# Kernel optimization log

Measured on AMD Instinct MI355X. Metric: run time of the kernel, lower is better.

Reference implementation:

```python
import jax, jax.numpy as jnp
import numpy as np
from jax import lax

B, T, V, E, H = 256, 512, 128, 64, 256


def lstm_cell(x, h, c, Wih, Whh, bih, bhh):
    # PyTorch gate order: i, f, g, o
    gates = x @ Wih.T + h @ Whh.T + bih + bhh
    i, f, g, o = jnp.split(gates, 4, axis=-1)
    c_new = jax.nn.sigmoid(f) * c + jax.nn.sigmoid(i) * jnp.tanh(g)
    h_new = jax.nn.sigmoid(o) * jnp.tanh(c_new)
    return h_new, c_new


def setup_inputs() -> dict:
    key = jax.random.key(0)
    ks = jax.random.split(key, 16)
    s = 0.05
    emb = jax.random.normal(ks[1], (V, E), jnp.float32) * s
    emb = emb.at[0].set(0.0)  # padding_idx=0
    return {
        "x": jax.random.randint(ks[0], (B, T), 0, V),
        "emb": emb,
        "Wih_e": jax.random.normal(ks[2], (4 * H, E), jnp.float32) * s,
        "Whh_e": jax.random.normal(ks[3], (4 * H, H), jnp.float32) * s,
        "bih_e": jax.random.normal(ks[4], (4 * H,), jnp.float32) * s,
        "bhh_e": jax.random.normal(ks[5], (4 * H,), jnp.float32) * s,
        "Wq": jax.random.normal(ks[6], (H, H), jnp.float32) * s,
        "Wk": jax.random.normal(ks[7], (H, H), jnp.float32) * s,
        "v": jax.random.normal(ks[8], (H,), jnp.float32) * s,
        "Wih_d": jax.random.normal(ks[9], (4 * H, E + H), jnp.float32) * s,
        "Whh_d": jax.random.normal(ks[10], (4 * H, H), jnp.float32) * s,
        "bih_d": jax.random.normal(ks[11], (4 * H,), jnp.float32) * s,
        "bhh_d": jax.random.normal(ks[12], (4 * H,), jnp.float32) * s,
        "Wfc": jax.random.normal(ks[13], (V, H), jnp.float32) * s,
        "bfc": jax.random.normal(ks[14], (V,), jnp.float32) * s,
    }


def reference(x, emb, Wih_e, Whh_e, bih_e, bhh_e, Wq, Wk, v,
              Wih_d, Whh_d, bih_d, bhh_d, Wfc, bfc):
    Bx = x.shape[0]
    embedded = emb[x]                          # (B, T, E)  (dropout in eval mode = identity)
    emb_tbE = embedded.transpose(1, 0, 2)      # (T, B, E)

    # ---- Encoder LSTM ----
    h0 = jnp.zeros((Bx, H), embedded.dtype)
    c0 = jnp.zeros((Bx, H), embedded.dtype)

    def enc_step(carry, x_t):
        h, c = carry
        h, c = lstm_cell(x_t, h, c, Wih_e, Whh_e, bih_e, bhh_e)
        return (h, c), h

    (h_n, c_n), enc_seq = lax.scan(enc_step, (h0, c0), emb_tbE)
    enc_out = enc_seq.transpose(1, 0, 2)       # (B, T, H)

    # ---- Attention precompute ----
    keys_proj = enc_out @ Wk.T                 # (B, T, H)
    pad_mask = (x == 0)                        # (B, T)

    # ---- Decoder loop (teacher forcing) ----
    def dec_step(carry, emb_t):
        h, c = carry
        q = h @ Wq.T                                        # (B, H)
        energy = jnp.tanh(q[:, None, :] + keys_proj) @ v    # (B, T)
        energy = jnp.where(pad_mask, -1e9, energy)
        w = jax.nn.softmax(energy, axis=-1)
        context = jnp.einsum('bt,bth->bh', w, enc_out)      # (B, H)
        dec_in = jnp.concatenate([emb_t, context], axis=-1)  # (B, E+H)
        h, c = lstm_cell(dec_in, h, c, Wih_d, Whh_d, bih_d, bhh_d)
        return (h, c), h

    (h_f, c_f), dec_seq = lax.scan(dec_step, (h_n, c_n), emb_tbE)
    logits = dec_seq.transpose(1, 0, 2) @ Wfc.T + bfc       # (B, T, V)
    return logits, h_f, c_f
```

## Files before the change

### kernel.cpp

```cpp
#include <hip/hip_runtime.h>
#include <hip/hip_bf16.h>
#include <stdint.h>

#define NB 256
#define NT 512
#define NV 128
#define NE 64
#define NH 256

typedef __fp16 h2t __attribute__((ext_vector_type(2)));

__device__ __forceinline__ float lo_bf(unsigned u){ return __uint_as_float(u << 16); }
__device__ __forceinline__ float hi_bf(unsigned u){ return __uint_as_float(u & 0xffff0000u); }
__device__ __forceinline__ unsigned short f2us(float f){
  unsigned u = __float_as_uint(f);
  unsigned r = u + 0x7fffu + ((u >> 16) & 1u);
  return (unsigned short)(r >> 16);
}
__device__ __forceinline__ float sigm(float x){
  return __builtin_amdgcn_rcpf(1.f + __expf(-x));
}
__device__ __forceinline__ float ftanh(float xx){
  float a = fabsf(xx);
  a = fminf(a, 9.f);
  float e = __expf(2.f * a);
  float r = __builtin_amdgcn_rcpf(e + 1.f);
  float t = (e - 1.f) * r;
  return copysignf(t, xx);
}
__device__ __forceinline__ unsigned pkf16(float a, float b){
  h2t h = __builtin_amdgcn_cvt_pkrtz(a, b);
  unsigned u; __builtin_memcpy(&u, &h, 4); return u;
}
__device__ __forceinline__ float fdot2(unsigned a, unsigned b, float c){
#if __has_builtin(__builtin_amdgcn_fdot2)
  h2t A, B; __builtin_memcpy(&A, &a, 4); __builtin_memcpy(&B, &b, 4);
  return __builtin_amdgcn_fdot2(A, B, c, false);
#else
  h2t A, B; __builtin_memcpy(&A, &a, 4); __builtin_memcpy(&B, &b, 4);
  return c + (float)A.x*(float)B.x + (float)A.y*(float)B.y;
#endif
}

__global__ __launch_bounds__(256, 1)
void prep_kernel(const float* __restrict__ Wq, const float* __restrict__ Wfc,
                 const float* __restrict__ Wihd, const float* __restrict__ Whhd,
                 const float* __restrict__ Wihe, const float* __restrict__ Whhe,
                 const float* __restrict__ Wk,
                 unsigned* __restrict__ Wq4, unsigned* __restrict__ Wfc4,
                 unsigned* __restrict__ Wihd4, unsigned* __restrict__ Whhd4,
                 unsigned* __restrict__ Wihe4, unsigned* __restrict__ Whhe4,
                 unsigned* __restrict__ Wke4)
{
  const int blk = blockIdx.x, tid = threadIdx.x;
  if (blk < 64){
    int k2p = blk;
    #pragma unroll
    for (int l = 0; l < 2; ++l){
      int i = l*256 + tid, c = i>>1, j = i&1, k = 4*k2p + 2*j;
      Wq4[k2p*512 + i] = pkf16(Wq[c*256 + k], Wq[c*256 + k + 1]);
    }
  } else if (blk < 128){
    int k2p = blk - 64;
    int c = tid>>1, j = tid&1, k = 4*k2p + 2*j;
    Wfc4[k2p*256 + tid] = pkf16(Wfc[c*256 + k], Wfc[c*256 + k + 1]);
  } else if (blk < 208){
    int k2p = blk - 128;
    #pragma unroll
    for (int l = 0; l < 8; ++l){
      int i = l*256 + tid, g = i>>1, j = i&1, k = 4*k2p + 2*j;
      Wihd4[(size_t)k2p*2048 + i] = pkf16(Wihd[g*320 + k], Wihd[g*320 + k + 1]);
    }
  } else if (blk < 272){
    int k2p = blk - 208;
    #pragma unroll
    for (int l = 0; l < 8; ++l){
      int i = l*256 + tid, g = i>>1, j = i&1, k = 4*k2p + 2*j;
      Whhd4[(size_t)k2p*2048 + i] = pkf16(Whhd[g*256 + k], Whhd[g*256 + k + 1]);
    }
  } else if (blk < 288){
    int k2p = blk - 272;
    #pragma unroll
    for (int l = 0; l < 8; ++l){
      int i = l*256 + tid, g = i>>1, j = i&1, k = 4*k2p + 2*j;
      Wihe4[(size_t)k2p*2048 + i] = pkf16(Wihe[g*64 + k], Wihe[g*64 + k + 1]);
    }
  } else if (blk < 352){
    int k2p = blk - 288;
    #pragma unroll
    for (int l = 0; l < 8; ++l){
      int i = l*256 + tid, g = i>>1, j = i&1, k = 4*k2p + 2*j;
      Whhe4[(size_t)k2p*2048 + i] = pkf16(Whhe[g*256 + k], Whhe[g*256 + k + 1]);
    }
  } else {
    int k2p = blk - 352;
    #pragma unroll
    for (int l = 0; l < 2; ++l){
      int i = l*256 + tid, c = i>>1, j = i&1, k = 4*k2p + 2*j;
      Wke4[k2p*512 + i] = pkf16(Wk[c*256 + k], Wk[c*256 + k + 1]);
    }
  }
}

__global__ __launch_bounds__(256, 1)
void tr_kernel(const unsigned short* __restrict__ keys_n, unsigned short* __restrict__ keys_t)
{
  __shared__ unsigned short tile[64][68];
  const int blk = blockIdx.x, tid = threadIdx.x;
  const int b  = blk >> 5;
  const int tt = (blk >> 2) & 7;
  const int hh = blk & 3;
  const int t0 = tt*64, h0 = hh*64;

  #pragma unroll
  for (int i = 0; i < 4; ++i){
    int idx = tid + i*256;
    int t = idx >> 4, h4 = (idx & 15)*4;
    uint2 u = *(const uint2*)(keys_n + ((size_t)b*NT + t0 + t)*NH + h0 + h4);
    *(uint2*)&tile[t][h4] = u;
  }
  __syncthreads();
  #pragma unroll
  for (int i = 0; i < 4; ++i){
    int idx = tid + i*256;
    int h = idx >> 4, t4 = (idx & 15)*4;
    unsigned short a = tile[t4+0][h], bb = tile[t4+1][h], cc = tile[t4+2][h], dd = tile[t4+3][h];
    uint2 u; u.x = (unsigned)a | ((unsigned)bb << 16); u.y = (unsigned)cc | ((unsigned)dd << 16);
    *(uint2*)(keys_t + ((size_t)b*NH + h0 + h)*NT + t0 + t4) = u;
  }
}

__global__ __launch_bounds__(1024, 1)
void enc_kernel(const int* __restrict__ x, const float* __restrict__ emb,
                const unsigned* __restrict__ Wihe4, const unsigned* __restrict__ Whhe4,
                const float* __restrict__ bih, const float* __restrict__ bhh,
                const unsigned* __restrict__ Wke4,
                unsigned short* __restrict__ enc_out, unsigned short* __restrict__ keys_n,
                float* __restrict__ g_h, float* __restrict__ g_c)
{
  const int tid = threadIdx.x;
  const int b0  = blockIdx.x * 2;

  __shared__ unsigned sH2[2][128];
  __shared__ unsigned sXe2[2][32];
  __shared__ float sG[2][1024];
  __shared__ float sBias[1024];
  __shared__ float sKP[1024];
  __shared__ uint8_t sXi[2][512];

  sBias[tid] = bih[tid] + bhh[tid];
  { int r = tid >> 9; sXi[r][tid & 511] = (uint8_t)x[(b0 + r)*NT + (tid & 511)]; }
  if (tid < 256) sH2[tid>>7][tid&127] = 0u;
  __syncthreads();
  if (tid < 64){
    int r = tid>>5, p = tid&31, idx = sXi[r][0];
    sXe2[r][p] = pkf16(emb[idx*NE + 2*p], emb[idx*NE + 2*p + 1]);
  }
  float creg = 0.f, hl = 0.f;
  __syncthreads();

  for (int t = 0; t < NT; ++t){
    {
      const int g = tid;
      float a0 = sBias[g], a1 = a0;
      const unsigned* Wi = Wihe4 + g*2;
      #pragma unroll 4
      for (int p = 0; p < 16; ++p){
        uint2 w = *(const uint2*)(Wi + (size_t)p*2048);
        a0 = fdot2(sXe2[0][2*p], w.x, a0); a0 = fdot2(sXe2[0][2*p+1], w.y, a0);
        a1 = fdot2(sXe2[1][2*p], w.x, a1); a1 = fdot2(sXe2[1][2*p+1], w.y, a1);
      }
      const unsigned* Wh = Whhe4 + g*2;
      #pragma unroll 4
      for (int p = 0; p < 64; ++p){
        uint2 w = *(const uint2*)(Wh + (size_t)p*2048);
        a0 = fdot2(sH2[0][2*p], w.x, a0); a0 = fdot2(sH2[0][2*p+1], w.y, a0);
        a1 = fdot2(sH2[1][2*p], w.x, a1); a1 = fdot2(sH2[1][2*p+1], w.y, a1);
      }
      sG[0][g] = a0; sG[1][g] = a1;
    }
    if (t > 0){
      const int r = tid>>9, half = (tid>>8)&1, c = tid&255;
      float kp = 0.f;
      const unsigned* Wk4 = Wke4 + c*2;
      #pragma unroll 4
      for (int p = 0; p < 32; ++p){
        int k2p = half*32 + p;
        uint2 w = *(const uint2*)(Wk4 + k2p*512);
        kp = fdot2(sH2[r][2*k2p], w.x, kp);
        kp = fdot2(sH2[r][2*k2p+1], w.y, kp);
      }
      sKP[tid] = kp;
    }
    __syncthreads();
    if (tid < 512){
      const int r = tid>>8, cc = tid&255;
      float gi = sigm (sG[r][cc]);
      float gf = sigm (sG[r][256+cc]);
      float gg = ftanh(sG[r][512+cc]);
      float go = sigm (sG[r][768+cc]);
      float cn = gf*creg + gi*gg;
      float hn = go*ftanh(cn);
      creg = cn; hl = hn;
      enc_out[((size_t)(b0+r)*NT + t)*NH + cc] = f2us(hn);
      float hb = __shfl_down(hn, 1, 64);
      if (!(cc & 1)) sH2[r][cc>>1] = pkf16(hn, hb);
      if (tid < 64 && (t+1) < NT){
        int r2 = tid>>5, p = tid&31, idx = sXi[r2][t+1];
        sXe2[r2][p] = pkf16(emb[idx*NE + 2*p], emb[idx*NE + 2*p + 1]);
      }
    } else if (t > 0){
      const int r = (tid>>8)&1, c = tid&255;
      float kv = sKP[(r<<9) + c] + sKP[(r<<9) + 256 + c];
      keys_n[((size_t)(b0+r)*NT + (t-1))*NH + c] = f2us(kv);
    }
    __syncthreads();
  }
  {
    const int r = tid>>9, half = (tid>>8)&1, c = tid&255;
    float kp = 0.f;
    const unsigned* Wk4 = Wke4 + c*2;
    #pragma unroll 4
    for (int p = 0; p < 32; ++p){
      int k2p = half*32 + p;
      uint2 w = *(const uint2*)(Wk4 + k2p*512);
      kp = fdot2(sH2[r][2*k2p], w.x, kp);
      kp = fdot2(sH2[r][2*k2p+1], w.y, kp);
    }
    sKP[tid] = kp;
  }
  __syncthreads();
  if (tid >= 512){
    const int r = (tid>>8)&1, c = tid&255;
    float kv = sKP[(r<<9) + c] + sKP[(r<<9) + 256 + c];
    keys_n[((size_t)(b0+r)*NT + (NT-1))*NH + c] = f2us(kv);
  } else {
    const int r = tid>>8, cc = tid&255;
    g_h[(b0+r)*NH + cc] = hl;
    g_c[(b0+r)*NH + cc] = creg;
  }
}

__global__ __launch_bounds__(1024, 1)
void dec_kernel(const int* __restrict__ x, const float* __restrict__ emb,
                const unsigned* __restrict__ Wq4, const float* __restrict__ vvec,
                const unsigned* __restrict__ Wihd4, const unsigned* __restrict__ Whhd4,
                const float* __restrict__ bih, const float* __restrict__ bhh,
                const unsigned short* __restrict__ enc_out, const unsigned short* __restrict__ keys_t,
                const float* __restrict__ g_h, const float* __restrict__ g_c,
                unsigned* __restrict__ h2_hist, float* __restrict__ out_h, float* __restrict__ out_c)
{
  const int tid = threadIdx.x;
  const int b   = blockIdx.x;

  extern __shared__ unsigned short sKpin[];

  __shared__ float sTMP[4096];
  __shared__ float sWp[512];
  __shared__ float sRed[8];
  __shared__ float sQ2[256];
  __shared__ unsigned sH2[128];
  __shared__ unsigned sCtx2[128];
  __shared__ unsigned sXe2[32];
  __shared__ float sG[1024];
  __shared__ float sBiasD[1024];
  __shared__ float sVm2[256];
  __shared__ float sVs[8];
  __shared__ uint8_t sXi[512];

  sBiasD[tid] = bih[tid] + bhh[tid];
  if (tid < 256) sVm2[tid] = -2.f * vvec[tid];
  if (tid < 512) sXi[tid] = (uint8_t)x[b*NT + tid];
  if (tid < 128) sH2[tid] = pkf16(g_h[b*NH + 2*tid], g_h[b*NH + 2*tid + 1]);
  if (tid < 8){
    float s = 0.f;
    #pragma unroll
    for (int j = 0; j < 12; ++j) s += vvec[tid*12 + j];
    #pragma unroll
    for (int j = 0; j < 20; ++j) s += vvec[96 + tid*20 + j];
    sVs[tid] = s;
  }
  {
    const unsigned* src = (const unsigned*)(keys_t + (size_t)b*NH*NT);
    unsigned* dst = (unsigned*)sKpin;
    #pragma unroll
    for (int i = 0; i < 24; ++i) dst[tid + i*1024] = src[tid + i*1024];
  }
  float creg = (tid < 256) ? g_c[b*NH + tid] : 0.f;
  float hl = 0.f;
  const float CLN = 2.885390081777927f;
  __syncthreads();

  for (int t = 0; t < NT; ++t){
    {
      const int c = tid & 255, kq = tid >> 8;
      float a = 0.f;
      const unsigned* Wp = Wq4 + c*2;
      #pragma unroll 4
      for (int p = 0; p < 16; ++p){
        int k2p = kq*16 + p;
        uint2 w = *(const uint2*)(Wp + k2p*512);
        a = fdot2(sH2[2*k2p], w.x, a);
        a = fdot2(sH2[2*k2p+1], w.y, a);
      }
      sTMP[kq*256 + c] = a;
    }
    __syncthreads();
    if (tid < 256){
      float qv = sTMP[tid] + sTMP[256 + tid] + sTMP[512 + tid] + sTMP[768 + tid];
      sQ2[tid] = CLN * qv;
    } else if (tid < 288){
      int p = tid - 256, idx = sXi[t];
      sXe2[p] = pkf16(emb[idx*NE + 2*p], emb[idx*NE + 2*p + 1]);
    }
    __syncthreads();
    {
      const int kh = tid >> 7, sp = tid & 127;
      float e0 = sVs[kh], e1 = e0, e2 = e0, e3 = e0;
      const unsigned short* ktg = keys_t + ((size_t)b*NH + 96 + kh*20)*NT + sp*4;
      #pragma unroll 4
      for (int j = 0; j < 20; ++j){
        uint2 u = *(const uint2*)(ktg + (size_t)j*NT);
        int ka = 96 + kh*20 + j;
        float q2 = sQ2[ka];
        float vm = sVm2[ka];
        float r0 = __builtin_amdgcn_rcpf(1.f + exp2f(fmaf(CLN, lo_bf(u.x), q2)));
        float r1 = __builtin_amdgcn_rcpf(1.f + exp2f(fmaf(CLN, hi_bf(u.x), q2)));
        float r2 = __builtin_amdgcn_rcpf(1.f + exp2f(fmaf(CLN, lo_bf(u.y), q2)));
        float r3 = __builtin_amdgcn_rcpf(1.f + exp2f(fmaf(CLN, hi_bf(u.y), q2)));
        e0 = fmaf(vm, r0, e0); e1 = fmaf(vm, r1, e1);
        e2 = fmaf(vm, r2, e2); e3 = fmaf(vm, r3, e3);
      }
      const unsigned short* ktl = sKpin + (size_t)(kh*12)*NT + sp*4;
      #pragma unroll 4
      for (int j = 0; j < 12; ++j){
        uint2 u = *(const uint2*)(ktl + (size_t)j*NT);
        int ka = kh*12 + j;
        float q2 = sQ2[ka];
        float vm = sVm2[ka];
        float r0 = __builtin_amdgcn_rcpf(1.f + exp2f(fmaf(CLN, lo_bf(u.x), q2)));
        float r1 = __builtin_amdgcn_rcpf(1.f + exp2f(fmaf(CLN, hi_bf(u.x), q2)));
        float r2 = __builtin_amdgcn_rcpf(1.f + exp2f(fmaf(CLN, lo_bf(u.y), q2)));
        float r3 = __builtin_amdgcn_rcpf(1.f + exp2f(fmaf(CLN, hi_bf(u.y), q2)));
        e0 = fmaf(vm, r0, e0); e1 = fmaf(vm, r1, e1);
        e2 = fmaf(vm, r2, e2); e3 = fmaf(vm, r3, e3);
      }
      *(float4*)(sTMP + kh*512 + sp*4) = make_float4(e0,e1,e2,e3);
    }
    __syncthreads();
    if (tid < 512){
      float e = sTMP[tid]      + sTMP[512+tid]  + sTMP[1024+tid] + sTMP[1536+tid]
              + sTMP[2048+tid] + sTMP[2560+tid] + sTMP[3072+tid] + sTMP[3584+tid];
      float w = (sXi[tid] == 0) ? 0.f : __expf(e);
      sWp[tid] = w;
      float s = w;
      #pragma unroll
      for (int off = 32; off > 0; off >>= 1) s += __shfl_down(s, off, 64);
      if ((tid & 63) == 0) sRed[tid >> 6] = s;
    }
    __syncthreads();
    {
      const int sc = tid >> 6;
      const int kc = tid & 63;
      const unsigned short* ep = enc_out + ((size_t)b*NT + sc*32)*NH + kc*4;
      float a0=0.f, a1=0.f, a2=0.f, a3=0.f;
      #pragma unroll 8
      for (int ss = 0; ss < 32; ++ss){
        float w = sWp[sc*32 + ss];
        uint2 u = *(const uint2*)(ep + (size_t)ss*NH);
        a0 += w*lo_bf(u.x); a1 += w*hi_bf(u.x);
        a2 += w*lo_bf(u.y); a3 += w*hi_bf(u.y);
      }
      *(float4*)(sTMP + sc*256 + kc*4) = make_float4(a0,a1,a2,a3);
    }
    __syncthreads();
    if (tid < 256){
      float den = sRed[0]+sRed[1]+sRed[2]+sRed[3]+sRed[4]+sRed[5]+sRed[6]+sRed[7];
      float rden = (den > 0.f) ? (1.f/den) : 0.f;
      float cs = 0.f;
      #pragma unroll
      for (int p = 0; p < 16; ++p) cs += sTMP[p*256 + tid];
      float cv = cs * rden;
      float cb = __shfl_down(cv, 1, 64);
      if (!(tid & 1)) sCtx2[tid>>1] = pkf16(cv, cb);
    }
    __syncthreads();
    {
      const int g = tid;
      float a = sBiasD[g];
      const unsigned* Wi = Wihd4 + g*2;
      #pragma unroll 4
      for (int p = 0; p < 16; ++p){
        uint2 w = *(const uint2*)(Wi + (size_t)p*2048);
        a = fdot2(sXe2[2*p], w.x, a); a = fdot2(sXe2[2*p+1], w.y, a);
      }
      #pragma unroll 4
      for (int p = 0; p < 64; ++p){
        uint2 w = *(const uint2*)(Wi + (size_t)(16+p)*2048);
        a = fdot2(sCtx2[2*p], w.x, a); a = fdot2(sCtx2[2*p+1], w.y, a);
      }
      const unsigned* Wh = Whhd4 + g*2;
      #pragma unroll 4
      for (int p = 0; p < 64; ++p){
        uint2 w = *(const uint2*)(Wh + (size_t)p*2048);
        a = fdot2(sH2[2*p], w.x, a); a = fdot2(sH2[2*p+1], w.y, a);
      }
      sG[g] = a;
    }
    __syncthreads();
    if (tid < 256){
      float gi = sigm (sG[tid]);
      float gf = sigm (sG[256 + tid]);
      float gg = ftanh(sG[512 + tid]);
      float go = sigm (sG[768 + tid]);
      float cn = gf*creg + gi*gg;
      float hn = go*ftanh(cn);
      creg = cn; hl = hn;
      float hb = __shfl_down(hn, 1, 64);
      if (!(tid & 1)){
        unsigned hp = pkf16(hn, hb);
        sH2[tid>>1] = hp;
        h2_hist[((size_t)b*NT + t)*128 + (tid>>1)] = hp;
      }
    }
    __syncthreads();
  }

  if (tid < 256){
    out_h[b*NH + tid] = hl;
    out_c[b*NH + tid] = creg;
  }
}

__global__ __launch_bounds__(256, 1)
void fc_kernel(const unsigned* __restrict__ h2_hist, const unsigned* __restrict__ Wfc4,
               const float* __restrict__ bfc, float* __restrict__ logits)
{
  __shared__ unsigned sHH[1024];
  const int tid = threadIdx.x;
  const size_t row0 = (size_t)blockIdx.x * 8;
  #pragma unroll
  for (int l = 0; l < 4; ++l) sHH[l*256 + tid] = h2_hist[row0*128 + l*256 + tid];
  __syncthreads();
  const int r = tid >> 7, v = tid & 127;
  float bv = bfc[v];
  float a0 = bv, a1 = bv, a2 = bv, a3 = bv;
  const unsigned* Wp = Wfc4 + v*2;
  #pragma unroll 4
  for (int k2p = 0; k2p < 64; ++k2p){
    uint2 w = *(const uint2*)(Wp + k2p*256);
    int k2 = 2*k2p;
    a0 = fdot2(sHH[(r  )*128 + k2], w.x, a0); a0 = fdot2(sHH[(r  )*128 + k2+1], w.y, a0);
    a1 = fdot2(sHH[(r+2)*128 + k2], w.x, a1); a1 = fdot2(sHH[(r+2)*128 + k2+1], w.y, a1);
    a2 = fdot2(sHH[(r+4)*128 + k2], w.x, a2); a2 = fdot2(sHH[(r+4)*128 + k2+1], w.y, a2);
    a3 = fdot2(sHH[(r+6)*128 + k2], w.x, a3); a3 = fdot2(sHH[(r+6)*128 + k2+1], w.y, a3);
  }
  logits[(row0 + r    )*NV + v] = a0;
  logits[(row0 + r + 2)*NV + v] = a1;
  logits[(row0 + r + 4)*NV + v] = a2;
  logits[(row0 + r + 6)*NV + v] = a3;
}

extern "C" void kernel_launch(void* const* d_in, const int* in_sizes, int n_in,
                              void* d_out, int out_size, void* d_ws, size_t ws_size,
                              hipStream_t stream)
{
  (void)in_sizes; (void)n_in; (void)out_size; (void)ws_size;
  const int*   x    = (const int*)  d_in[0];
  const float* emb  = (const float*)d_in[1];
  const float* Wihe = (const float*)d_in[2];
  const float* Whhe = (const float*)d_in[3];
  const float* bihe = (const float*)d_in[4];
  const float* bhhe = (const float*)d_in[5];
  const float* Wq   = (const float*)d_in[6];
  const float* Wk   = (const float*)d_in[7];
  const float* vv   = (const float*)d_in[8];
  const float* Wihd = (const float*)d_in[9];
  const float* Whhd = (const float*)d_in[10];
  const float* bihd = (const float*)d_in[11];
  const float* bhhd = (const float*)d_in[12];
  const float* Wfc  = (const float*)d_in[13];
  const float* bfc  = (const float*)d_in[14];

  char* ws = (char*)d_ws;
  const size_t M64 = 67108864;
  unsigned short* enc   = (unsigned short*)(ws);
  unsigned short* keysn = (unsigned short*)(ws + M64);
  unsigned short* keyst = (unsigned short*)(ws + 2*M64);
  unsigned* h2_hist     = (unsigned*)(ws + M64);
  float* g_h = (float*)(ws + 3*M64);
  float* g_c = g_h + NB*NH;
  unsigned* Wq4   = (unsigned*)(g_c + NB*NH);
  unsigned* Wfc4  = Wq4   + 64*512;
  unsigned* Wihd4 = Wfc4  + 64*256;
  unsigned* Whhd4 = Wihd4 + 80*2048;
  unsigned* Wihe4 = Whhd4 + 64*2048;
  unsigned* Whhe4 = Wihe4 + 16*2048;
  unsigned* Wke4  = Whhe4 + 64*2048;

  float* out_logits = (float*)d_out;
  float* out_h = out_logits + (size_t)NB*NT*NV;
  float* out_c = out_h + NB*NH;

  const int dynLds = 96 * 512 * 2;
  static int attrSet = 0;
  if (!attrSet){
    hipFuncSetAttribute(reinterpret_cast<const void*>(dec_kernel),
                        hipFuncAttributeMaxDynamicSharedMemorySize, dynLds);
    attrSet = 1;
  }

  prep_kernel<<<dim3(416), dim3(256), 0, stream>>>(
      Wq, Wfc, Wihd, Whhd, Wihe, Whhe, Wk,
      Wq4, Wfc4, Wihd4, Whhd4, Wihe4, Whhe4, Wke4);
  enc_kernel<<<dim3(128), dim3(1024), 0, stream>>>(
      x, emb, Wihe4, Whhe4, bihe, bhhe, Wke4, enc, keysn, g_h, g_c);
  tr_kernel<<<dim3(8192), dim3(256), 0, stream>>>(keysn, keyst);
  dec_kernel<<<dim3(256), dim3(1024), dynLds, stream>>>(
      x, emb, Wq4, vv, Wihd4, Whhd4, bihd, bhhd,
      enc, keyst, g_h, g_c, h2_hist, out_h, out_c);
  fc_kernel<<<dim3(16384), dim3(256), 0, stream>>>(h2_hist, Wfc4, bfc, out_logits);
}
```

Before: 25.47 ms.

## Split decoder threads to overlap recurrent-gate matvec with attention phases

Threads 0-511 now compute the attention energies and context with 8-wide vector loads, instead of all 1024 threads doing 4-wide work. The other 512 threads compute the h·Whh and embedding·Wih parts of the gate pre-activations into a new shared buffer during those same phases. The final gate stage then only needs the context·Wih part. This hides the h-dependent matvec behind attention work and shortens the serial gate phase, at the cost of halving the threads available for the attention math.

After: 25.86 ms. Within noise of the previous version (+1.5%).

```diff
diff --git a/kernel.cpp b/kernel.cpp
--- a/kernel.cpp
+++ b/kernel.cpp
@@ -256,6 +256,7 @@
   extern __shared__ unsigned short sKpin[];
 
   __shared__ float sTMP[4096];
+  __shared__ float sGP[1024];
   __shared__ float sWp[512];
   __shared__ float sRed[8];
   __shared__ float sQ2[256];
@@ -292,6 +293,7 @@
   __syncthreads();
 
   for (int t = 0; t < NT; ++t){
+    float ga0 = 0.f, ga1 = 0.f;
     {
       const int c = tid & 255, kq = tid >> 8;
       float a = 0.f;
@@ -314,38 +316,50 @@
       sXe2[p] = pkf16(emb[idx*NE + 2*p], emb[idx*NE + 2*p + 1]);
     }
     __syncthreads();
-    {
-      const int kh = tid >> 7, sp = tid & 127;
-      float e0 = sVs[kh], e1 = e0, e2 = e0, e3 = e0;
-      const unsigned short* ktg = keys_t + ((size_t)b*NH + 96 + kh*20)*NT + sp*4;
-      #pragma unroll 4
+    if (tid < 512){
+      const int kh = tid >> 6, sp = tid & 63;
+      float e0 = sVs[kh], e1 = e0, e2 = e0, e3 = e0, e4 = e0, e5 = e0, e6 = e0, e7 = e0;
+      const unsigned short* ktg = keys_t + ((size_t)b*NH + 96 + kh*20)*NT + sp*8;
+      #pragma unroll 2
       for (int j = 0; j < 20; ++j){
-        uint2 u = *(const uint2*)(ktg + (size_t)j*NT);
+        uint4 u = *(const uint4*)(ktg + (size_t)j*NT);
         int ka = 96 + kh*20 + j;
-        float q2 = sQ2[ka];
-        float vm = sVm2[ka];
-        float r0 = __builtin_amdgcn_rcpf(1.f + exp2f(fmaf(CLN, lo_bf(u.x), q2)));
-        float r1 = __builtin_amdgcn_rcpf(1.f + exp2f(fmaf(CLN, hi_bf(u.x), q2)));
-        float r2 = __builtin_amdgcn_rcpf(1.f + exp2f(fmaf(CLN, lo_bf(u.y), q2)));
-        float r3 = __builtin_amdgcn_rcpf(1.f + exp2f(fmaf(CLN, hi_bf(u.y), q2)));
-        e0 = fmaf(vm, r0, e0); e1 = fmaf(vm, r1, e1);
-        e2 = fmaf(vm, r2, e2); e3 = fmaf(vm, r3, e3);
-      }
-      const unsigned short* ktl = sKpin + (size_t)(kh*12)*NT + sp*4;
-      #pragma unroll 4
+        float q2 = sQ2[ka], vm = sVm2[ka];
+        e0 = fmaf(vm, __builtin_amdgcn_rcpf(1.f + exp2f(fmaf(CLN, lo_bf(u.x), q2))), e0);
+        e1 = fmaf(vm, __builtin_amdgcn_rcpf(1.f + exp2f(fmaf(CLN, hi_bf(u.x), q2))), e1);
+        e2 = fmaf(vm, __builtin_amdgcn_rcpf(1.f + exp2f(fmaf(CLN, lo_bf(u.y), q2))), e2);
+        e3 = fmaf(vm, __builtin_amdgcn_rcpf(1.f + exp2f(fmaf(CLN, hi_bf(u.y), q2))), e3);
+        e4 = fmaf(vm, __builtin_amdgcn_rcpf(1.f + exp2f(fmaf(CLN, lo_bf(u.z), q2))), e4);
+        e5 = fmaf(vm, __builtin_amdgcn_rcpf(1.f + exp2f(fmaf(CLN, hi_bf(u.z), q2))), e5);
+        e6 = fmaf(vm, __builtin_amdgcn_rcpf(1.f + exp2f(fmaf(CLN, lo_bf(u.w), q2))), e6);
+        e7 = fmaf(vm, __builtin_amdgcn_rcpf(1.f + exp2f(fmaf(CLN, hi_bf(u.w), q2))), e7);
+      }
+      const unsigned short* ktl = sKpin + (size_t)(kh*12)*NT + sp*8;
+      #pragma unroll 2
       for (int j = 0; j < 12; ++j){
-        uint2 u = *(const uint2*)(ktl + (size_t)j*NT);
+        uint4 u = *(const uint4*)(ktl + (size_t)j*NT);
         int ka = kh*12 + j;
-        float q2 = sQ2[ka];
-        float vm = sVm2[ka];
-        float r0 = __builtin_amdgcn_rcpf(1.f + exp2f(fmaf(CLN, lo_bf(u.x), q2)));
-        float r1 = __builtin_amdgcn_rcpf(1.f + exp2f(fmaf(CLN, hi_bf(u.x), q2)));
-        float r2 = __builtin_amdgcn_rcpf(1.f + exp2f(fmaf(CLN, lo_bf(u.y), q2)));
-        float r3 = __builtin_amdgcn_rcpf(1.f + exp2f(fmaf(CLN, hi_bf(u.y), q2)));
-        e0 = fmaf(vm, r0, e0); e1 = fmaf(vm, r1, e1);
-        e2 = fmaf(vm, r2, e2); e3 = fmaf(vm, r3, e3);
-      }
-      *(float4*)(sTMP + kh*512 + sp*4) = make_float4(e0,e1,e2,e3);
+        float q2 = sQ2[ka], vm = sVm2[ka];
+        e0 = fmaf(vm, __builtin_amdgcn_rcpf(1.f + exp2f(fmaf(CLN, lo_bf(u.x), q2))), e0);
+        e1 = fmaf(vm, __builtin_amdgcn_rcpf(1.f + exp2f(fmaf(CLN, hi_bf(u.x), q2))), e1);
+        e2 = fmaf(vm, __builtin_amdgcn_rcpf(1.f + exp2f(fmaf(CLN, lo_bf(u.y), q2))), e2);
+        e3 = fmaf(vm, __builtin_amdgcn_rcpf(1.f + exp2f(fmaf(CLN, hi_bf(u.y), q2))), e3);
+        e4 = fmaf(vm, __builtin_amdgcn_rcpf(1.f + exp2f(fmaf(CLN, lo_bf(u.z), q2))), e4);
+        e5 = fmaf(vm, __builtin_amdgcn_rcpf(1.f + exp2f(fmaf(CLN, hi_bf(u.z), q2))), e5);
+        e6 = fmaf(vm, __builtin_amdgcn_rcpf(1.f + exp2f(fmaf(CLN, lo_bf(u.w), q2))), e6);
+        e7 = fmaf(vm, __builtin_amdgcn_rcpf(1.f + exp2f(fmaf(CLN, hi_bf(u.w), q2))), e7);
+      }
+      *(float4*)(sTMP + kh*512 + sp*8)     = make_float4(e0,e1,e2,e3);
+      *(float4*)(sTMP + kh*512 + sp*8 + 4) = make_float4(e4,e5,e6,e7);
+    } else {
+      const int g4 = (tid - 512)*4;
+      #pragma unroll 4
+      for (int k2p = 0; k2p < 40; ++k2p){
+        uint4 w = *(const uint4*)(Whhd4 + (size_t)k2p*2048 + g4);
+        unsigned h0 = sH2[2*k2p], h1 = sH2[2*k2p+1];
+        ga0 = fdot2(h0, w.x, ga0); ga0 = fdot2(h1, w.y, ga0);
+        ga1 = fdot2(h0, w.z, ga1); ga1 = fdot2(h1, w.w, ga1);
+      }
     }
     __syncthreads();
     if (tid < 512){
@@ -357,21 +371,42 @@
       #pragma unroll
       for (int off = 32; off > 0; off >>= 1) s += __shfl_down(s, off, 64);
       if ((tid & 63) == 0) sRed[tid >> 6] = s;
-    }
-    __syncthreads();
-    {
-      const int sc = tid >> 6;
-      const int kc = tid & 63;
-      const unsigned short* ep = enc_out + ((size_t)b*NT + sc*32)*NH + kc*4;
-      float a0=0.f, a1=0.f, a2=0.f, a3=0.f;
-      #pragma unroll 8
+    } else {
+      const int g4 = (tid - 512)*4;
+      #pragma unroll 4
+      for (int k2p = 40; k2p < 64; ++k2p){
+        uint4 w = *(const uint4*)(Whhd4 + (size_t)k2p*2048 + g4);
+        unsigned h0 = sH2[2*k2p], h1 = sH2[2*k2p+1];
+        ga0 = fdot2(h0, w.x, ga0); ga0 = fdot2(h1, w.y, ga0);
+        ga1 = fdot2(h0, w.z, ga1); ga1 = fdot2(h1, w.w, ga1);
+      }
+      #pragma unroll 4
+      for (int k2p = 0; k2p < 16; ++k2p){
+        uint4 w = *(const uint4*)(Wihd4 + (size_t)k2p*2048 + g4);
+        unsigned x0 = sXe2[2*k2p], x1 = sXe2[2*k2p+1];
+        ga0 = fdot2(x0, w.x, ga0); ga0 = fdot2(x1, w.y, ga0);
+        ga1 = fdot2(x0, w.z, ga1); ga1 = fdot2(x1, w.w, ga1);
+      }
+      sGP[(tid-512)*2]     = ga0;
+      sGP[(tid-512)*2 + 1] = ga1;
+    }
+    __syncthreads();
+    if (tid < 512){
+      const int sc = tid >> 5;
+      const int kc = tid & 31;
+      const unsigned short* ep = enc_out + ((size_t)b*NT + sc*32)*NH + kc*8;
+      float a0=0.f,a1=0.f,a2=0.f,a3=0.f,a4=0.f,a5=0.f,a6=0.f,a7=0.f;
+      #pragma unroll 4
       for (int ss = 0; ss < 32; ++ss){
         float w = sWp[sc*32 + ss];
-        uint2 u = *(const uint2*)(ep + (size_t)ss*NH);
+        uint4 u = *(const uint4*)(ep + (size_t)ss*NH);
         a0 += w*lo_bf(u.x); a1 += w*hi_bf(u.x);
         a2 += w*lo_bf(u.y); a3 += w*hi_bf(u.y);
-      }
-      *(float4*)(sTMP + sc*256 + kc*4) = make_float4(a0,a1,a2,a3);
+        a4 += w*lo_bf(u.z); a5 += w*hi_bf(u.z);
+        a6 += w*lo_bf(u.w); a7 += w*hi_bf(u.w);
+      }
+      *(float4*)(sTMP + sc*256 + kc*8)     = make_float4(a0,a1,a2,a3);
+      *(float4*)(sTMP + sc*256 + kc*8 + 4) = make_float4(a4,a5,a6,a7);
     }
     __syncthreads();
     if (tid < 256){
@@ -387,23 +422,13 @@
     __syncthreads();
     {
       const int g = tid;
-      float a = sBiasD[g];
-      const unsigned* Wi = Wihd4 + g*2;
-      #pragma unroll 4
-      for (int p = 0; p < 16; ++p){
-        uint2 w = *(const uint2*)(Wi + (size_t)p*2048);
-        a = fdot2(sXe2[2*p], w.x, a); a = fdot2(sXe2[2*p+1], w.y, a);
-      }
-      #pragma unroll 4
-      for (int p = 0; p < 64; ++p){
-        uint2 w = *(const uint2*)(Wi + (size_t)(16+p)*2048);
-        a = fdot2(sCtx2[2*p], w.x, a); a = fdot2(sCtx2[2*p+1], w.y, a);
-      }
-      const unsigned* Wh = Whhd4 + g*2;
-      #pragma unroll 4
-      for (int p = 0; p < 64; ++p){
-        uint2 w = *(const uint2*)(Wh + (size_t)p*2048);
-        a = fdot2(sH2[2*p], w.x, a); a = fdot2(sH2[2*p+1], w.y, a);
+      float a = sBiasD[g] + sGP[g];
+      const unsigned* Wc = Wihd4 + g*2;
+      #pragma unroll 4
+      for (int k2p = 16; k2p < 80; ++k2p){
+        uint2 w = *(const uint2*)(Wc + (size_t)k2p*2048);
+        a = fdot2(sCtx2[2*(k2p-16)], w.x, a);
+        a = fdot2(sCtx2[2*(k2p-16)+1], w.y, a);
       }
       sG[g] = a;
     }
```

## Process one batch row per encoder block and overlap key projection

Applied to the files above, without the earlier changes.

The encoder kernel now handles a single batch row per block and launches twice as many blocks, so per-step work shrinks and more compute units are used. The hidden state is double-buffered so the Wk key projection runs alongside the gate activation phase, removing the partial-sum shared buffer and its combine. The cost is that each block reloads the weights for only one row, which doubles total weight traffic.

New measurement: 25.23 ms (median of 2 runs). About the same (-0.9%).

```diff
diff --git a/kernel.cpp b/kernel.cpp
--- a/kernel.cpp
+++ b/kernel.cpp
@@ -139,105 +139,90 @@
                 float* __restrict__ g_h, float* __restrict__ g_c)
 {
   const int tid = threadIdx.x;
-  const int b0  = blockIdx.x * 2;
+  const int b   = blockIdx.x;
 
   __shared__ unsigned sH2[2][128];
-  __shared__ unsigned sXe2[2][32];
-  __shared__ float sG[2][1024];
+  __shared__ unsigned sXe2[32];
+  __shared__ float sG[1024];
   __shared__ float sBias[1024];
-  __shared__ float sKP[1024];
-  __shared__ uint8_t sXi[2][512];
+  __shared__ uint8_t sXi[512];
 
   sBias[tid] = bih[tid] + bhh[tid];
-  { int r = tid >> 9; sXi[r][tid & 511] = (uint8_t)x[(b0 + r)*NT + (tid & 511)]; }
-  if (tid < 256) sH2[tid>>7][tid&127] = 0u;
+  if (tid < 512) sXi[tid] = (uint8_t)x[b*NT + tid];
+  if (tid < 128){ sH2[0][tid] = 0u; sH2[1][tid] = 0u; }
   __syncthreads();
-  if (tid < 64){
-    int r = tid>>5, p = tid&31, idx = sXi[r][0];
-    sXe2[r][p] = pkf16(emb[idx*NE + 2*p], emb[idx*NE + 2*p + 1]);
+  if (tid < 32){
+    int idx = sXi[0];
+    sXe2[tid] = pkf16(emb[idx*NE + 2*tid], emb[idx*NE + 2*tid + 1]);
   }
   float creg = 0.f, hl = 0.f;
   __syncthreads();
 
   for (int t = 0; t < NT; ++t){
+    const int cur = t & 1, nxt = cur ^ 1;
     {
       const int g = tid;
-      float a0 = sBias[g], a1 = a0;
+      float a = sBias[g];
       const unsigned* Wi = Wihe4 + g*2;
       #pragma unroll 4
       for (int p = 0; p < 16; ++p){
         uint2 w = *(const uint2*)(Wi + (size_t)p*2048);
-        a0 = fdot2(sXe2[0][2*p], w.x, a0); a0 = fdot2(sXe2[0][2*p+1], w.y, a0);
-        a1 = fdot2(sXe2[1][2*p], w.x, a1); a1 = fdot2(sXe2[1][2*p+1], w.y, a1);
+        a = fdot2(sXe2[2*p], w.x, a); a = fdot2(sXe2[2*p+1], w.y, a);
       }
       const unsigned* Wh = Whhe4 + g*2;
       #pragma unroll 4
       for (int p = 0; p < 64; ++p){
         uint2 w = *(const uint2*)(Wh + (size_t)p*2048);
-        a0 = fdot2(sH2[0][2*p], w.x, a0); a0 = fdot2(sH2[0][2*p+1], w.y, a0);
-        a1 = fdot2(sH2[1][2*p], w.x, a1); a1 = fdot2(sH2[1][2*p+1], w.y, a1);
-      }
-      sG[0][g] = a0; sG[1][g] = a1;
-    }
-    if (t > 0){
-      const int r = tid>>9, half = (tid>>8)&1, c = tid&255;
-      float kp = 0.f;
-      const unsigned* Wk4 = Wke4 + c*2;
-      #pragma unroll 4
-      for (int p = 0; p < 32; ++p){
-        int k2p = half*32 + p;
-        uint2 w = *(const uint2*)(Wk4 + k2p*512);
-        kp = fdot2(sH2[r][2*k2p], w.x, kp);
-        kp = fdot2(sH2[r][2*k2p+1], w.y, kp);
-      }
-      sKP[tid] = kp;
-    }
-    __syncthreads();
-    if (tid < 512){
-      const int r = tid>>8, cc = tid&255;
-      float gi = sigm (sG[r][cc]);
-      float gf = sigm (sG[r][256+cc]);
-      float gg = ftanh(sG[r][512+cc]);
-      float go = sigm (sG[r][768+cc]);
+        a = fdot2(sH2[cur][2*p], w.x, a); a = fdot2(sH2[cur][2*p+1], w.y, a);
+      }
+      sG[g] = a;
+    }
+    __syncthreads();
+    if (tid < 256){
+      float gi = sigm (sG[tid]);
+      float gf = sigm (sG[256 + tid]);
+      float gg = ftanh(sG[512 + tid]);
+      float go = sigm (sG[768 + tid]);
       float cn = gf*creg + gi*gg;
       float hn = go*ftanh(cn);
       creg = cn; hl = hn;
-      enc_out[((size_t)(b0+r)*NT + t)*NH + cc] = f2us(hn);
+      enc_out[((size_t)b*NT + t)*NH + tid] = f2us(hn);
       float hb = __shfl_down(hn, 1, 64);
-      if (!(cc & 1)) sH2[r][cc>>1] = pkf16(hn, hb);
-      if (tid < 64 && (t+1) < NT){
-        int r2 = tid>>5, p = tid&31, idx = sXi[r2][t+1];
-        sXe2[r2][p] = pkf16(emb[idx*NE + 2*p], emb[idx*NE + 2*p + 1]);
-      }
-    } else if (t > 0){
-      const int r = (tid>>8)&1, c = tid&255;
-      float kv = sKP[(r<<9) + c] + sKP[(r<<9) + 256 + c];
-      keys_n[((size_t)(b0+r)*NT + (t-1))*NH + c] = f2us(kv);
-    }
-    __syncthreads();
-  }
-  {
-    const int r = tid>>9, half = (tid>>8)&1, c = tid&255;
+      if (!(tid & 1)) sH2[nxt][tid>>1] = pkf16(hn, hb);
+    } else if (tid < 512){
+      if (t > 0){
+        const int c = tid - 256;
+        float kp = 0.f;
+        const unsigned* Wk4 = Wke4 + c*2;
+        #pragma unroll 4
+        for (int k2p = 0; k2p < 64; ++k2p){
+          uint2 w = *(const uint2*)(Wk4 + k2p*512);
+          kp = fdot2(sH2[cur][2*k2p], w.x, kp);
+          kp = fdot2(sH2[cur][2*k2p+1], w.y, kp);
+        }
+        keys_n[((size_t)b*NT + (t-1))*NH + c] = f2us(kp);
+      }
+    } else if (tid < 544 && (t+1) < NT){
+      int p = tid - 512, idx = sXi[t+1];
+      sXe2[p] = pkf16(emb[idx*NE + 2*p], emb[idx*NE + 2*p + 1]);
+    }
+    __syncthreads();
+  }
+
+  if (tid >= 256 && tid < 512){
+    const int c = tid - 256;
     float kp = 0.f;
     const unsigned* Wk4 = Wke4 + c*2;
     #pragma unroll 4
-    for (int p = 0; p < 32; ++p){
-      int k2p = half*32 + p;
+    for (int k2p = 0; k2p < 64; ++k2p){
       uint2 w = *(const uint2*)(Wk4 + k2p*512);
-      kp = fdot2(sH2[r][2*k2p], w.x, kp);
-      kp = fdot2(sH2[r][2*k2p+1], w.y, kp);
-    }
-    sKP[tid] = kp;
-  }
-  __syncthreads();
-  if (tid >= 512){
-    const int r = (tid>>8)&1, c = tid&255;
-    float kv = sKP[(r<<9) + c] + sKP[(r<<9) + 256 + c];
-    keys_n[((size_t)(b0+r)*NT + (NT-1))*NH + c] = f2us(kv);
-  } else {
-    const int r = tid>>8, cc = tid&255;
-    g_h[(b0+r)*NH + cc] = hl;
-    g_c[(b0+r)*NH + cc] = creg;
+      kp = fdot2(sH2[0][2*k2p], w.x, kp);
+      kp = fdot2(sH2[0][2*k2p+1], w.y, kp);
+    }
+    keys_n[((size_t)b*NT + (NT-1))*NH + c] = f2us(kp);
+  } else if (tid < 256){
+    g_h[b*NH + tid] = hl;
+    g_c[b*NH + tid] = creg;
   }
 }
 
@@ -513,7 +498,7 @@
   prep_kernel<<<dim3(416), dim3(256), 0, stream>>>(
       Wq, Wfc, Wihd, Whhd, Wihe, Whhe, Wk,
       Wq4, Wfc4, Wihd4, Whhd4, Wihe4, Whhe4, Wke4);
-  enc_kernel<<<dim3(128), dim3(1024), 0, stream>>>(
+  enc_kernel<<<dim3(256), dim3(1024), 0, stream>>>(
       x, emb, Wihe4, Whhe4, bihe, bhhe, Wke4, enc, keysn, g_h, g_c);
   tr_kernel<<<dim3(8192), dim3(256), 0, stream>>>(keysn, keyst);
   dec_kernel<<<dim3(256), dim3(1024), dynLds, stream>>>(
```
